# Performance work log

Hardware: AMD Instinct MI355X
Metric: run time of the kernel (lower is better)

The kernel has to match this reference:

```python
import jax, jax.numpy as jnp
import numpy as np

B, C, H, D, W = 1, 32, 32, 32, 32   # batch, channels, 3D grid
M1 = M2 = M3 = 16                   # fourier modes kept per dim
KS = 3                              # spatial attention kernel size
MEM = 5                             # memory slots
EPS = 1e-5
N = H * D * W


def _gelu(x):
    return jax.nn.gelu(x, approximate=False)  # torch exact GELU


def _gn(x):
    # GroupNorm(1, C) without affine: normalize over (C,H,D,W) per sample
    mu = jnp.mean(x, axis=(1, 2, 3, 4), keepdims=True)
    var = jnp.var(x, axis=(1, 2, 3, 4), keepdims=True)
    return (x - mu) * jax.lax.rsqrt(var + EPS)


def _spectral_conv(x, wr, wi):
    # classic 3D FNO spectral conv: keep low modes (4 corner blocks in dims H,D; low block in rfft dim W)
    xf = jnp.fft.rfftn(x, axes=(2, 3, 4))                 # (B,C,H,D,W//2+1) complex64
    w = wr + 1j * wi                                      # (4,Cin,Cout,M1,M2,M3)
    of = jnp.zeros((x.shape[0], C, H, D, W // 2 + 1), xf.dtype)
    corners = [(slice(0, M1), slice(0, M2)), (slice(H - M1, H), slice(0, M2)),
               (slice(0, M1), slice(D - M2, D)), (slice(H - M1, H), slice(D - M2, D))]
    for i, (s1, s2) in enumerate(corners):
        of = of.at[:, :, s1, s2, :M3].set(
            jnp.einsum('bixyz,ioxyz->boxyz', xf[:, :, s1, s2, :M3], w[i]))
    return jnp.fft.irfftn(of, s=(H, D, W), axes=(2, 3, 4))


def _forward(x, t, prev_memory, w_spec_r, w_spec_i, norm1_g, norm1_b,
             mlp_w1, mlp_b1, mlp_w2, mlp_b2, tin_gw, tin_gb, tin_bw, tin_bb,
             q_w, q_b, k_w, k_b, v_w, v_b, mem_key, mem_value,
             gate_w, gate_b, gru_wih, gru_whh, gru_bih, gru_bhh):
    skip1 = x
    skip2 = _gelu(x)
    # spectral conv -> GroupNorm(affine) + residual -> gelu
    h = _spectral_conv(x, w_spec_r, w_spec_i)
    h = _gelu(_gn(h) * norm1_g[None, :, None, None, None]
              + norm1_b[None, :, None, None, None] + skip1)
    # pointwise Conv1d MLP over channels
    hf = h.reshape(B, C, N)
    u = _gelu(jnp.einsum('oc,bcn->bon', mlp_w1, hf) + mlp_b1[None, :, None])
    hf = jnp.einsum('oc,bcn->bon', mlp_w2, u) + mlp_b2[None, :, None]
    h = hf.reshape(B, C, H, D, W)
    # time-conditioned instance norm: gamma/beta from 1x1 conv over t (B,C)
    gamma = (jnp.einsum('oc,bc->bo', tin_gw, t) + tin_gb)[:, :, None, None, None]
    beta = (jnp.einsum('oc,bc->bo', tin_bw, t) + tin_bb)[:, :, None, None, None]
    h = gamma * _gn(h) + beta
    # ---- spatial attention with memory ----
    pad = KS // 2
    xp = jnp.pad(h, ((0, 0), (0, 0), (pad, pad), (pad, pad), (pad, pad)))
    # 3D unfold: (B,C,27,N) patches via 27 shifted views
    patches = jnp.stack([xp[:, :, i:i + H, j:j + D, l:l + W]
                         for i in range(KS) for j in range(KS) for l in range(KS)],
                        axis=2).reshape(B, C, KS ** 3, N)
    hf = h.reshape(B, C, N)
    q = jnp.einsum('oc,bcn->bon', q_w, hf) + q_b[None, :, None]              # (B,C,N)
    k_sp = jnp.einsum('oc,bcmn->bomn', k_w, patches) + k_b[None, :, None, None]
    v_sp = jnp.einsum('oc,bcmn->bomn', v_w, patches) + v_b[None, :, None, None]
    mem_k = jnp.broadcast_to(mem_key[None, :, :, None], (B, C, MEM, N))
    mem_v = jnp.broadcast_to(mem_value[None, :, :, None], (B, C, MEM, N))
    k = jnp.concatenate([mem_k, k_sp], axis=2)                               # (B,C,32,N)
    v = jnp.concatenate([mem_v, v_sp], axis=2)
    attn = jax.nn.softmax(q[:, :, None, :] * k / jnp.sqrt(jnp.float32(C)), axis=2)
    out = jnp.sum(attn * v, axis=2)                                          # (B,C,N)
    cat = jnp.concatenate([hf, out], axis=1)                                 # (B,2C,N)
    gate = jax.nn.sigmoid(jnp.einsum('oc,bcn->bon', gate_w, cat) + gate_b[None, :, None])
    out = gate * out + (1.0 - gate) * hf
    out = out.reshape(B, C, H, D, W)
    # GRUCell memory update from spatially pooled features
    m_in = jnp.mean(out, axis=(2, 3, 4))                                     # (B,C)
    gi = m_in @ gru_wih.T + gru_bih
    gh = prev_memory @ gru_whh.T + gru_bhh
    ir, iz, inn = jnp.split(gi, 3, axis=1)
    hr, hz, hn = jnp.split(gh, 3, axis=1)
    r = jax.nn.sigmoid(ir + hr)
    z = jax.nn.sigmoid(iz + hz)
    n = jnp.tanh(inn + r * hn)
    new_memory = (1.0 - z) * n + z * prev_memory                             # (B,C)
    return out + skip2, new_memory


def setup_inputs():
    key = jax.random.key(0)
    ks = jax.random.split(key, 20)
    def rn(k, shape, s):
        return jax.random.normal(k, shape, jnp.float32) * s
    spec_scale = 1.0 / (C * C)
    return dict(
        x=jax.random.normal(ks[0], (B, C, H, D, W), jnp.float32),
        t=jax.random.normal(ks[1], (B, C), jnp.float32),
        prev_memory=jnp.zeros((B, C), jnp.float32),
        w_spec_r=rn(ks[2], (4, C, C, M1, M2, M3), spec_scale),
        w_spec_i=rn(ks[3], (4, C, C, M1, M2, M3), spec_scale),
        norm1_g=jnp.ones((C,), jnp.float32),
        norm1_b=jnp.zeros((C,), jnp.float32),
        mlp_w1=rn(ks[4], (C // 2, C), 0.1), mlp_b1=jnp.zeros((C // 2,), jnp.float32),
        mlp_w2=rn(ks[5], (C, C // 2), 0.1), mlp_b2=jnp.zeros((C,), jnp.float32),
        tin_gw=rn(ks[6], (C, C), 0.1), tin_gb=jnp.ones((C,), jnp.float32),
        tin_bw=rn(ks[7], (C, C), 0.1), tin_bb=jnp.zeros((C,), jnp.float32),
        q_w=rn(ks[8], (C, C), 0.1), q_b=jnp.zeros((C,), jnp.float32),
        k_w=rn(ks[9], (C, C), 0.1), k_b=jnp.zeros((C,), jnp.float32),
        v_w=rn(ks[10], (C, C), 0.1), v_b=jnp.zeros((C,), jnp.float32),
        mem_key=jax.random.normal(ks[11], (C, MEM), jnp.float32),
        mem_value=jax.random.normal(ks[12], (C, MEM), jnp.float32),
        gate_w=rn(ks[13], (C, 2 * C), 0.1), gate_b=jnp.zeros((C,), jnp.float32),
        gru_wih=rn(ks[14], (3 * C, C), 0.1), gru_whh=rn(ks[15], (3 * C, C), 0.1),
        gru_bih=jnp.zeros((3 * C,), jnp.float32), gru_bhh=jnp.zeros((3 * C,), jnp.float32),
    )


def reference(x, t, prev_memory, w_spec_r, w_spec_i, norm1_g, norm1_b,
              mlp_w1, mlp_b1, mlp_w2, mlp_b2, tin_gw, tin_gb, tin_bw, tin_bb,
              q_w, q_b, k_w, k_b, v_w, v_b, mem_key, mem_value,
              gate_w, gate_b, gru_wih, gru_whh, gru_bih, gru_bhh):
    return _forward(x, t, prev_memory, w_spec_r, w_spec_i, norm1_g, norm1_b,
                    mlp_w1, mlp_b1, mlp_w2, mlp_b2, tin_gw, tin_gb, tin_bw, tin_bb,
                    q_w, q_b, k_w, k_b, v_w, v_b, mem_key, mem_value,
                    gate_w, gate_b, gru_wih, gru_whh, gru_bih, gru_bhh)
```

## Files before the change

kernel.cpp:

```cpp
#include <hip/hip_runtime.h>
#include <hip/hip_bf16.h>
#include <math.h>

#define NSP 32768
#define NZ 17

__device__ __forceinline__ float geluf(float x){
    return 0.5f * x * (1.0f + erff(x * 0.70710678118654752f));
}
__device__ __forceinline__ float sigmoidf_(float x){
    return 1.0f / (1.0f + __expf(-x));
}


__global__ void k_fwd(const float* __restrict__ x, float* __restrict__ Br, float* __restrict__ Bi){
    __shared__ float tile[32*33];
    __shared__ float ar[544], ai[544];
    __shared__ float ct[32], st[32];
    int b = blockIdx.x, t = threadIdx.x;
    if (t < 32){ float ang = 6.283185307179586477f * (float)t / 32.0f; ct[t] = cosf(ang); st[t] = sinf(ang); }
    const float* src = x + b * 1024;
    for (int j = t; j < 1024; j += 256) tile[(j & 31) * 33 + (j >> 5)] = src[j];
    __syncthreads();
    for (int idx = t; idx < 544; idx += 256){
        int d = idx / 17, z = idx - d * 17;
        float sr = 0.f, si = 0.f;
        #pragma unroll
        for (int w = 0; w < 32; ++w){
            int a = (z * w) & 31;
            float v = tile[w * 33 + d];
            sr += v * ct[a];
            si -= v * st[a];
        }
        ar[idx] = sr; ai[idx] = si;
    }
    __syncthreads();
    for (int idx = t; idx < 544; idx += 256){
        int kd = idx / 17, z = idx - kd * 17;
        float sr = 0.f, si = 0.f;
        #pragma unroll
        for (int d = 0; d < 32; ++d){
            int a = (kd * d) & 31;
            float c = ct[a], s = st[a];
            float vr = ar[d * 17 + z], vi = ai[d * 17 + z];
            sr += vr * c + vi * s;
            si += vi * c - vr * s;
        }
        Br[b * 544 + idx] = sr; Bi[b * 544 + idx] = si;
    }
}

__global__ void k_fft_h(const float* __restrict__ Br, const float* __restrict__ Bi,
                        float* __restrict__ Ar, float* __restrict__ Ai){
    __shared__ float ir[544], ii[544];
    __shared__ float ct[32], st[32];
    int b = blockIdx.x, t = threadIdx.x;
    int c = b >> 5, d = b & 31;
    if (t < 32){ float ang = 6.283185307179586477f * (float)t / 32.0f; ct[t] = cosf(ang); st[t] = sinf(ang); }
    for (int j = t; j < 544; j += 256){
        int h = j / 17, z = j - h * 17;
        int g = ((c * 32 + h) * 32 + d) * NZ + z;
        ir[j] = Br[g]; ii[j] = Bi[g];
    }
    __syncthreads();
    for (int idx = t; idx < 544; idx += 256){
        int kh = idx / 17, z = idx - kh * 17;
        float sr = 0.f, si = 0.f;
        #pragma unroll
        for (int h = 0; h < 32; ++h){
            int a = (kh * h) & 31;
            float c2 = ct[a], s2 = st[a];
            float vr = ir[h * 17 + z], vi = ii[h * 17 + z];
            sr += vr * c2 + vi * s2;
            si += vi * c2 - vr * s2;
        }
        int g = ((c * 32 + kh) * 32 + d) * NZ + z;
        Ar[g] = sr; Ai[g] = si;
    }
}

__global__ void k_modemul(const float* __restrict__ Xr, const float* __restrict__ Xi,
                          const float* __restrict__ Wr, const float* __restrict__ Wi,
                          float* __restrict__ Or, float* __restrict__ Oi){
    __shared__ float xr[32 * 64], xi[32 * 64];
    int b = blockIdx.x;
    int corner = b >> 6;
    int xm = (b >> 2) & 15;
    int ymg = b & 3;
    int xg = xm + ((corner & 1) << 4);
    int ybase = ymg * 4 + ((corner >> 1) << 4);
    int t = threadIdx.x;
    for (int idx = t; idx < 2048; idx += 256){
        int i = idx >> 6, m = idx & 63;
        int y = ybase + (m >> 4), z = m & 15;
        int g = ((i * 32 + xg) * 32 + y) * NZ + z;
        xr[idx] = Xr[g]; xi[idx] = Xi[g];
    }
    if (t < 128){
        int o = t >> 2, y = ybase + (t & 3);
        int g = ((o * 32 + xg) * 32 + y) * NZ + 16;
        Or[g] = 0.f; Oi[g] = 0.f;
    }
    __syncthreads();
    int wv = t >> 6, lane = t & 63;
    float ar[8], ai[8];
    #pragma unroll
    for (int oo = 0; oo < 8; ++oo){ ar[oo] = 0.f; ai[oo] = 0.f; }
    int wtail = xm * 256 + ymg * 64 + lane;
    for (int i = 0; i < 32; ++i){
        float vxr = xr[i * 64 + lane], vxi = xi[i * 64 + lane];
        #pragma unroll
        for (int oo = 0; oo < 8; ++oo){
            int o = oo * 4 + wv;
            int addr = ((corner * 32 + i) * 32 + o) * 4096 + wtail;
            float wr = Wr[addr], wi = Wi[addr];
            ar[oo] += wr * vxr - wi * vxi;
            ai[oo] += wr * vxi + wi * vxr;
        }
    }
    int y = ybase + (lane >> 4), z = lane & 15;
    #pragma unroll
    for (int oo = 0; oo < 8; ++oo){
        int o = oo * 4 + wv;
        int g = ((o * 32 + xg) * 32 + y) * NZ + z;
        Or[g] = ar[oo]; Oi[g] = ai[oo];
    }
}

__global__ void k_ifft_h(const float* __restrict__ Br, const float* __restrict__ Bi,
                         float* __restrict__ Ar, float* __restrict__ Ai){
    __shared__ float ir[544], ii[544];
    __shared__ float ct[32], st[32];
    int b = blockIdx.x, t = threadIdx.x;
    int c = b >> 5, y = b & 31;
    if (t < 32){ float ang = 6.283185307179586477f * (float)t / 32.0f; ct[t] = cosf(ang); st[t] = sinf(ang); }
    for (int j = t; j < 544; j += 256){
        int xk = j / 17, z = j - xk * 17;
        int g = ((c * 32 + xk) * 32 + y) * NZ + z;
        ir[j] = Br[g]; ii[j] = Bi[g];
    }
    __syncthreads();
    for (int idx = t; idx < 544; idx += 256){
        int h = idx / 17, z = idx - h * 17;
        float sr = 0.f, si = 0.f;
        #pragma unroll
        for (int k = 0; k < 32; ++k){
            int a = (k * h) & 31;
            float c2 = ct[a], s2 = st[a];
            float vr = ir[k * 17 + z], vi = ii[k * 17 + z];
            sr += vr * c2 - vi * s2;
            si += vr * s2 + vi * c2;
        }
        int g = ((c * 32 + h) * 32 + y) * NZ + z;
        Ar[g] = sr; Ai[g] = si;
    }
}

__global__ void k_inv(const float* __restrict__ Ar, const float* __restrict__ Ai,
                      float* __restrict__ spec,
                      float* __restrict__ psum, float* __restrict__ psq){
    __shared__ float ir[544], ii[544];
    __shared__ float cr[544], ci[544];
    __shared__ float ct[32], st[32];
    __shared__ float ls[256], lq[256];
    int b = blockIdx.x, t = threadIdx.x;
    if (t < 32){ float ang = 6.283185307179586477f * (float)t / 32.0f; ct[t] = cosf(ang); st[t] = sinf(ang); }
    const float* pr = Ar + b * 544;
    const float* pi = Ai + b * 544;
    for (int j = t; j < 544; j += 256){ ir[j] = pr[j]; ii[j] = pi[j]; }
    __syncthreads();
    for (int idx = t; idx < 544; idx += 256){
        int d = idx / 17, z = idx - d * 17;
        float sr = 0.f, si = 0.f;
        #pragma unroll
        for (int k = 0; k < 32; ++k){
            int a = (k * d) & 31;
            float c2 = ct[a], s2 = st[a];
            float vr = ir[k * 17 + z], vi = ii[k * 17 + z];
            sr += vr * c2 - vi * s2;
            si += vr * s2 + vi * c2;
        }
        cr[idx] = sr; ci[idx] = si;
    }
    __syncthreads();
    const float inv = 1.0f / 32768.0f;
    float s_loc = 0.f, q_loc = 0.f;
    for (int idx = t; idx < 1024; idx += 256){
        int d = idx >> 5, w = idx & 31;
        float s = cr[d * 17 + 0] + ((w & 1) ? -cr[d * 17 + 16] : cr[d * 17 + 16]);
        #pragma unroll
        for (int z = 1; z < 16; ++z){
            int a = (z * w) & 31;
            s += 2.0f * (cr[d * 17 + z] * ct[a] - ci[d * 17 + z] * st[a]);
        }
        s *= inv;
        spec[b * 1024 + idx] = s;
        s_loc += s; q_loc += s * s;
    }
    ls[t] = s_loc; lq[t] = q_loc; __syncthreads();
    for (int off = 128; off > 0; off >>= 1){
        if (t < off){ ls[t] += ls[t + off]; lq[t] += lq[t + off]; }
        __syncthreads();
    }
    if (t == 0){ psum[b] = ls[0]; psq[b] = lq[0]; }
}


__global__ void k_finalize1(const float* __restrict__ psum, const float* __restrict__ psq,
                            int n, float* __restrict__ red){
    __shared__ float ls[256], lq[256];
    int t = threadIdx.x;
    float s = 0.f, q = 0.f;
    for (int j = t; j < n; j += 256){ s += psum[j]; q += psq[j]; }
    ls[t] = s; lq[t] = q; __syncthreads();
    for (int off = 128; off > 0; off >>= 1){
        if (t < off){ ls[t] += ls[t + off]; lq[t] += lq[t + off]; }
        __syncthreads();
    }
    if (t == 0){
        float mu = ls[0] * (1.0f / 1048576.0f);
        float var = lq[0] * (1.0f / 1048576.0f) - mu * mu;
        red[0] = mu; red[1] = rsqrtf(var + 1e-5f);
    }
}

__global__ void k_finalize2(const float* __restrict__ psum, const float* __restrict__ psq,
                            int n, const float* __restrict__ tin,
                            const float* __restrict__ tgw, const float* __restrict__ tgb,
                            const float* __restrict__ tbw, const float* __restrict__ tbb,
                            float* __restrict__ red){
    __shared__ float ls[256], lq[256];
    int t = threadIdx.x;
    float s = 0.f, q = 0.f;
    for (int j = t; j < n; j += 256){ s += psum[j]; q += psq[j]; }
    ls[t] = s; lq[t] = q; __syncthreads();
    for (int off = 128; off > 0; off >>= 1){
        if (t < off){ ls[t] += ls[t + off]; lq[t] += lq[t + off]; }
        __syncthreads();
    }
    if (t == 0){
        float mu = ls[0] * (1.0f / 1048576.0f);
        float var = lq[0] * (1.0f / 1048576.0f) - mu * mu;
        red[2] = mu; red[3] = rsqrtf(var + 1e-5f);
    }
    if (t < 64){
        int o = t & 31;
        const float* w = (t < 32) ? tgw : tbw;
        const float* bi = (t < 32) ? tgb : tbb;
        float a = bi[o];
        #pragma unroll
        for (int c = 0; c < 32; ++c) a += w[o * 32 + c] * tin[c];
        red[(t < 32 ? 16 : 48) + o] = a;
    }
}

__global__ void k_mlp(const float* __restrict__ spec, const float* __restrict__ x,
                      const float* __restrict__ n1g, const float* __restrict__ n1b,
                      const float* __restrict__ red,
                      const float* __restrict__ w1, const float* __restrict__ b1,
                      const float* __restrict__ w2, const float* __restrict__ b2,
                      float* __restrict__ h2,
                      float* __restrict__ psum, float* __restrict__ psq){
    __shared__ float W1[512], W2[512], B1[16], B2[32], GG[32], BB[32];
    __shared__ float ls[256], lq[256];
    int t = threadIdx.x;
    for (int j = t; j < 512; j += 256){ W1[j] = w1[j]; W2[j] = w2[j]; }
    if (t < 16) B1[t] = b1[t];
    if (t < 32){ B2[t] = b2[t]; GG[t] = n1g[t]; BB[t] = n1b[t]; }
    __syncthreads();
    float mu = red[0], rs = red[1];
    int n = blockIdx.x * 256 + t;
    float hv[32];
    #pragma unroll
    for (int c = 0; c < 32; ++c){
        float v = (spec[c * NSP + n] - mu) * rs * GG[c] + BB[c] + x[c * NSP + n];
        hv[c] = geluf(v);
    }
    float u[16];
    #pragma unroll
    for (int o = 0; o < 16; ++o){
        float a = B1[o];
        #pragma unroll
        for (int c = 0; c < 32; ++c) a += W1[o * 32 + c] * hv[c];
        u[o] = geluf(a);
    }
    float s_loc = 0.f, q_loc = 0.f;
    #pragma unroll
    for (int o = 0; o < 32; ++o){
        float a = B2[o];
        #pragma unroll
        for (int c = 0; c < 16; ++c) a += W2[o * 16 + c] * u[c];
        h2[o * NSP + n] = a;
        s_loc += a; q_loc += a * a;
    }
    ls[t] = s_loc; lq[t] = q_loc; __syncthreads();
    for (int off = 128; off > 0; off >>= 1){
        if (t < off){ ls[t] += ls[t + off]; lq[t] += lq[t + off]; }
        __syncthreads();
    }
    if (t == 0){ psum[blockIdx.x] = ls[0]; psq[blockIdx.x] = lq[0]; }
}

__global__ void k_qkv(const float* __restrict__ h2, const float* __restrict__ red,
                      const float* __restrict__ qw, const float* __restrict__ qb,
                      const float* __restrict__ kw, const float* __restrict__ vw,
                      float* __restrict__ h3, float* __restrict__ Q,
                      float* __restrict__ KH, float* __restrict__ VH){
    __shared__ float QW[1024], KW[1024], VW[1024], GA[32], BE[32], QB[32];
    int t = threadIdx.x;
    for (int j = t; j < 1024; j += 256){ QW[j] = qw[j]; KW[j] = kw[j]; VW[j] = vw[j]; }
    if (t < 32){ GA[t] = red[16 + t]; BE[t] = red[48 + t]; QB[t] = qb[t]; }
    __syncthreads();
    float mu = red[2], rs = red[3];
    int n = blockIdx.x * 256 + t;
    float hv[32];
    #pragma unroll
    for (int c = 0; c < 32; ++c){
        float v = GA[c] * ((h2[c * NSP + n] - mu) * rs) + BE[c];
        hv[c] = v;
        h3[c * NSP + n] = v;
    }
    #pragma unroll
    for (int o = 0; o < 32; ++o){
        float aq = QB[o], ak = 0.f, av = 0.f;
        #pragma unroll
        for (int c = 0; c < 32; ++c){
            float v = hv[c];
            aq += QW[o * 32 + c] * v;
            ak += KW[o * 32 + c] * v;
            av += VW[o * 32 + c] * v;
        }
        Q[o * NSP + n] = aq;
        KH[o * NSP + n] = ak;
        VH[o * NSP + n] = av;
    }
}

__global__ void k_attn(const float* __restrict__ Q, const float* __restrict__ KH,
                       const float* __restrict__ VH, const float* __restrict__ h3,
                       const float* __restrict__ x,
                       const float* __restrict__ kb, const float* __restrict__ vb,
                       const float* __restrict__ mk, const float* __restrict__ mv,
                       const float* __restrict__ gw, const float* __restrict__ gb,
                       float* __restrict__ outp, float* __restrict__ mpart){
    __shared__ float GWT1[1024], GWT2[1024];
    __shared__ float MK[160], MV[160];
    __shared__ float l_out[256], l_h3[256], l_fin[256];
    int t = threadIdx.x;
    for (int j = t; j < 1024; j += 256){
        int c_ = j & 31, cc_ = j >> 5;
        GWT1[j] = gw[c_ * 64 + cc_];
        GWT2[j] = gw[c_ * 64 + 32 + cc_];
    }
    if (t < 160){ MK[t] = mk[t]; MV[t] = mv[t]; }
    int bid = blockIdx.x;
    int swz = (bid & 7) * 512 + (bid >> 3);
    int c = t >> 3, nl = t & 7;
    int n = swz * 8 + nl;
    int w_ = n & 31, d_ = (n >> 5) & 31, h_ = n >> 10;
    const float scale = 0.17677669529663688f;
    float q = Q[c * NSP + n];
    float kbc = kb[c], vbc = vb[c];
    __syncthreads();
    float s = 0.f, acc = 0.f;
    #pragma unroll
    for (int j = 0; j < 5; ++j){
        float e = __expf(q * MK[c * 5 + j] * scale);
        s += e; acc += e * MV[c * 5 + j];
    }
    int oob = 0;
    for (int di = -1; di <= 1; ++di){
        int hh = h_ + di;
        if ((unsigned)hh >= 32u){ oob += 9; continue; }
        for (int dj = -1; dj <= 1; ++dj){
            int dd = d_ + dj;
            if ((unsigned)dd >= 32u){ oob += 3; continue; }
            int rbase = (hh * 32 + dd) * 32;
            #pragma unroll
            for (int dl = -1; dl <= 1; ++dl){
                int ww = w_ + dl;
                if ((unsigned)ww < 32u){
                    int np = rbase + ww;
                    float k = kbc + KH[c * NSP + np];
                    float v = vbc + VH[c * NSP + np];
                    float e = __expf(q * k * scale);
                    s += e; acc += e * v;
                } else oob++;
            }
        }
    }
    float eb = __expf(q * kbc * scale);
    s += (float)oob * eb; acc += (float)oob * eb * vbc;
    float out0 = acc / s;
    float h3v = h3[c * NSP + n];
    l_out[t] = out0;
    l_h3[t] = h3v;
    __syncthreads();
    float g = gb[c];
    #pragma unroll
    for (int cc = 0; cc < 32; ++cc){
        g += GWT1[cc * 32 + c] * l_h3[cc * 8 + nl] + GWT2[cc * 32 + c] * l_out[cc * 8 + nl];
    }
    g = sigmoidf_(g);
    float fin = g * out0 + (1.0f - g) * h3v;
    l_fin[t] = fin;
    float xo = x[c * NSP + n];
    outp[c * NSP + n] = fin + geluf(xo);
    __syncthreads();
    if (nl == 0){
        float ssum = 0.f;
        #pragma unroll
        for (int j = 0; j < 8; ++j) ssum += l_fin[c * 8 + j];
        mpart[c * 4096 + swz] = ssum;
    }
}

__global__ void k_mred(const float* __restrict__ mpart, float* __restrict__ red){
    __shared__ float ls[256];
    int c = blockIdx.x, t = threadIdx.x;
    const float4* p = (const float4*)(mpart + c * 4096);
    float s = 0.f;
    #pragma unroll
    for (int j = 0; j < 4; ++j){
        float4 v = p[t + j * 256];
        s += v.x + v.y + v.z + v.w;
    }
    ls[t] = s; __syncthreads();
    for (int off = 128; off > 0; off >>= 1){
        if (t < off) ls[t] += ls[t + off];
        __syncthreads();
    }
    if (t == 0) red[128 + c] = ls[0] * (1.0f / 32768.0f);
}

__global__ void k_gru(const float* __restrict__ red, const float* __restrict__ pm,
                      const float* __restrict__ wih, const float* __restrict__ whh,
                      const float* __restrict__ bih, const float* __restrict__ bhh,
                      float* __restrict__ outp){
    __shared__ float m_in[32], gi[96], gh[96];
    int t = threadIdx.x;
    if (t < 32) m_in[t] = red[128 + t];
    __syncthreads();
    if (t < 96){
        float a = bih[t], b2 = bhh[t];
        #pragma unroll
        for (int cc = 0; cc < 32; ++cc){
            a += wih[t * 32 + cc] * m_in[cc];
            b2 += whh[t * 32 + cc] * pm[cc];
        }
        gi[t] = a; gh[t] = b2;
    }
    __syncthreads();
    if (t < 32){
        float r = sigmoidf_(gi[t] + gh[t]);
        float z = sigmoidf_(gi[32 + t] + gh[32 + t]);
        float nn = tanhf(gi[64 + t] + r * gh[64 + t]);
        float nm = (1.0f - z) * nn + z * pm[t];
        outp[1048576 + t] = nm;
    }
}

extern "C" void kernel_launch(void* const* d_in, const int* in_sizes, int n_in,
                              void* d_out, int out_size, void* d_ws, size_t ws_size,
                              hipStream_t stream){
    const float* x   = (const float*)d_in[0];
    const float* tin = (const float*)d_in[1];
    const float* pm  = (const float*)d_in[2];
    const float* wsr = (const float*)d_in[3];
    const float* wsi = (const float*)d_in[4];
    const float* n1g = (const float*)d_in[5];
    const float* n1b = (const float*)d_in[6];
    const float* mw1 = (const float*)d_in[7];
    const float* mb1 = (const float*)d_in[8];
    const float* mw2 = (const float*)d_in[9];
    const float* mb2 = (const float*)d_in[10];
    const float* tgw = (const float*)d_in[11];
    const float* tgb = (const float*)d_in[12];
    const float* tbw = (const float*)d_in[13];
    const float* tbb = (const float*)d_in[14];
    const float* qw  = (const float*)d_in[15];
    const float* qb  = (const float*)d_in[16];
    const float* kw  = (const float*)d_in[17];
    const float* kb  = (const float*)d_in[18];
    const float* vw  = (const float*)d_in[19];
    const float* vb  = (const float*)d_in[20];
    const float* mk  = (const float*)d_in[21];
    const float* mv  = (const float*)d_in[22];
    const float* gw  = (const float*)d_in[23];
    const float* gb  = (const float*)d_in[24];
    const float* wih = (const float*)d_in[25];
    const float* whh = (const float*)d_in[26];
    const float* bih = (const float*)d_in[27];
    const float* bhh = (const float*)d_in[28];

    float* ws = (float*)d_ws;
    float* Ar   = ws + 0;
    float* Ai   = ws + 557056;
    float* Br   = ws + 1114112;
    float* Bi   = ws + 1671168;
    float* spec = ws + 2228224;
    float* h1   = ws + 3276800;
    float* h2   = ws + 4325376;
    float* h3   = ws + 5373952;
    float* red  = ws + 6422528;
    float* psum = ws + 6422784;
    float* psq  = ws + 6423808;
    float* Qb  = Br;
    float* KHb = spec;
    float* VHb = h1;
    float* mpart = Ar;

    float* outp = (float*)d_out;

    k_fwd    <<<1024, 256, 0, stream>>>(x, Br, Bi);
    k_fft_h  <<<1024, 256, 0, stream>>>(Br, Bi, Ar, Ai);
    k_modemul<<<256, 256, 0, stream>>>(Ar, Ai, wsr, wsi, Br, Bi);
    k_ifft_h <<<1024, 256, 0, stream>>>(Br, Bi, Ar, Ai);
    k_inv    <<<1024, 256, 0, stream>>>(Ar, Ai, spec, psum, psq);
    k_finalize1<<<1, 256, 0, stream>>>(psum, psq, 1024, red);
    k_mlp    <<<128, 256, 0, stream>>>(spec, x, n1g, n1b, red, mw1, mb1, mw2, mb2, h2, psum, psq);
    k_finalize2<<<1, 256, 0, stream>>>(psum, psq, 128, tin, tgw, tgb, tbw, tbb, red);
    k_qkv    <<<128, 256, 0, stream>>>(h2, red, qw, qb, kw, vw, h3, Qb, KHb, VHb);
    k_attn   <<<4096, 256, 0, stream>>>(Qb, KHb, VHb, h3, x, kb, vb, mk, mv, gw, gb, outp, mpart);
    k_mred   <<<32, 256, 0, stream>>>(mpart, red);
    k_gru    <<<1, 128, 0, stream>>>(red, pm, wih, whh, bih, bhh, outp);
}
```

Baseline: 197.7 us.

## Split attention into LDS-tiled neighbourhood kernel and separate per-point gate kernel

The fused attention kernel is split in two. The attention kernel now assigns one (channel, h-plane) pair per block and stages the three neighbouring K/V planes in shared memory, so the 27-point stencil reads LDS instead of repeatedly gathering from global memory. A new gate kernel keeps all 32 channels per spatial point in registers and computes the channel-mixing gate, the output and per-block channel sums for the memory mean. This adds an extra global round trip for the attention output and uses only 128 blocks for the gate kernel, which may leave many CUs idle.

```diff
diff --git a/kernel.cpp b/kernel.cpp
--- a/kernel.cpp
+++ b/kernel.cpp
@@ -337,96 +337,121 @@
 }
 
 __global__ void k_attn(const float* __restrict__ Q, const float* __restrict__ KH,
-                       const float* __restrict__ VH, const float* __restrict__ h3,
-                       const float* __restrict__ x,
+                       const float* __restrict__ VH,
                        const float* __restrict__ kb, const float* __restrict__ vb,
                        const float* __restrict__ mk, const float* __restrict__ mv,
+                       float* __restrict__ out0){
+    __shared__ float KL[3][1024], VL[3][1024];
+    int bid = blockIdx.x;
+    int swz = (bid & 7) * 128 + (bid >> 3);
+    int c = swz >> 5, h_ = swz & 31;
+    int t = threadIdx.x;
+    #pragma unroll
+    for (int p = 0; p < 3; ++p){
+        int hh = h_ - 1 + p;
+        if ((unsigned)hh < 32u){
+            const float* sk = KH + (c * 32 + hh) * 1024;
+            const float* sv = VH + (c * 32 + hh) * 1024;
+            for (int j = t; j < 1024; j += 256){ KL[p][j] = sk[j]; VL[p][j] = sv[j]; }
+        }
+    }
+    float kbc = kb[c], vbc = vb[c];
+    float mkv[5], mvv[5];
+    #pragma unroll
+    for (int j = 0; j < 5; ++j){ mkv[j] = mk[c * 5 + j]; mvv[j] = mv[c * 5 + j]; }
+    float qv[4];
+    #pragma unroll
+    for (int i = 0; i < 4; ++i) qv[i] = Q[c * NSP + h_ * 1024 + i * 256 + t];
+    __syncthreads();
+    const float scale = 0.17677669529663688f;
+    #pragma unroll
+    for (int i = 0; i < 4; ++i){
+        int nl = i * 256 + t;
+        int d_ = nl >> 5, w_ = nl & 31;
+        float q = qv[i];
+        float s = 0.f, acc = 0.f;
+        #pragma unroll
+        for (int j = 0; j < 5; ++j){
+            float e = __expf(q * mkv[j] * scale);
+            s += e; acc += e * mvv[j];
+        }
+        int oob = 0;
+        #pragma unroll
+        for (int p = 0; p < 3; ++p){
+            int hh = h_ - 1 + p;
+            if ((unsigned)hh >= 32u){ oob += 9; continue; }
+            #pragma unroll
+            for (int dj = -1; dj <= 1; ++dj){
+                int dd = d_ + dj;
+                if ((unsigned)dd >= 32u){ oob += 3; continue; }
+                int rb = dd * 32;
+                #pragma unroll
+                for (int dl = -1; dl <= 1; ++dl){
+                    int ww = w_ + dl;
+                    if ((unsigned)ww < 32u){
+                        float k = kbc + KL[p][rb + ww];
+                        float v = vbc + VL[p][rb + ww];
+                        float e = __expf(q * k * scale);
+                        s += e; acc += e * v;
+                    } else oob++;
+                }
+            }
+        }
+        float eb = __expf(q * kbc * scale);
+        s += (float)oob * eb; acc += (float)oob * eb * vbc;
+        out0[c * NSP + h_ * 1024 + nl] = acc / s;
+    }
+}
+
+__global__ void k_gate(const float* __restrict__ h3, const float* __restrict__ out0,
+                       const float* __restrict__ x,
                        const float* __restrict__ gw, const float* __restrict__ gb,
                        float* __restrict__ outp, float* __restrict__ mpart){
-    __shared__ float GWT1[1024], GWT2[1024];
-    __shared__ float MK[160], MV[160];
-    __shared__ float l_out[256], l_h3[256], l_fin[256];
-    int t = threadIdx.x;
-    for (int j = t; j < 1024; j += 256){
-        int c_ = j & 31, cc_ = j >> 5;
-        GWT1[j] = gw[c_ * 64 + cc_];
-        GWT2[j] = gw[c_ * 64 + 32 + cc_];
-    }
-    if (t < 160){ MK[t] = mk[t]; MV[t] = mv[t]; }
-    int bid = blockIdx.x;
-    int swz = (bid & 7) * 512 + (bid >> 3);
-    int c = t >> 3, nl = t & 7;
-    int n = swz * 8 + nl;
-    int w_ = n & 31, d_ = (n >> 5) & 31, h_ = n >> 10;
-    const float scale = 0.17677669529663688f;
-    float q = Q[c * NSP + n];
-    float kbc = kb[c], vbc = vb[c];
-    __syncthreads();
-    float s = 0.f, acc = 0.f;
-    #pragma unroll
-    for (int j = 0; j < 5; ++j){
-        float e = __expf(q * MK[c * 5 + j] * scale);
-        s += e; acc += e * MV[c * 5 + j];
-    }
-    int oob = 0;
-    for (int di = -1; di <= 1; ++di){
-        int hh = h_ + di;
-        if ((unsigned)hh >= 32u){ oob += 9; continue; }
-        for (int dj = -1; dj <= 1; ++dj){
-            int dd = d_ + dj;
-            if ((unsigned)dd >= 32u){ oob += 3; continue; }
-            int rbase = (hh * 32 + dd) * 32;
-            #pragma unroll
-            for (int dl = -1; dl <= 1; ++dl){
-                int ww = w_ + dl;
-                if ((unsigned)ww < 32u){
-                    int np = rbase + ww;
-                    float k = kbc + KH[c * NSP + np];
-                    float v = vbc + VH[c * NSP + np];
-                    float e = __expf(q * k * scale);
-                    s += e; acc += e * v;
-                } else oob++;
-            }
-        }
-    }
-    float eb = __expf(q * kbc * scale);
-    s += (float)oob * eb; acc += (float)oob * eb * vbc;
-    float out0 = acc / s;
-    float h3v = h3[c * NSP + n];
-    l_out[t] = out0;
-    l_h3[t] = h3v;
-    __syncthreads();
-    float g = gb[c];
-    #pragma unroll
-    for (int cc = 0; cc < 32; ++cc){
-        g += GWT1[cc * 32 + c] * l_h3[cc * 8 + nl] + GWT2[cc * 32 + c] * l_out[cc * 8 + nl];
-    }
-    g = sigmoidf_(g);
-    float fin = g * out0 + (1.0f - g) * h3v;
-    l_fin[t] = fin;
-    float xo = x[c * NSP + n];
-    outp[c * NSP + n] = fin + geluf(xo);
-    __syncthreads();
-    if (nl == 0){
-        float ssum = 0.f;
-        #pragma unroll
-        for (int j = 0; j < 8; ++j) ssum += l_fin[c * 8 + j];
-        mpart[c * 4096 + swz] = ssum;
+    __shared__ float GW[2048];
+    __shared__ float FT[32 * 264];
+    __shared__ float PS[256];
+    int t = threadIdx.x;
+    for (int j = t; j < 2048; j += 256) GW[j] = gw[j];
+    int n = blockIdx.x * 256 + t;
+    float hv[32], ov[32];
+    #pragma unroll
+    for (int c = 0; c < 32; ++c){ hv[c] = h3[c * NSP + n]; ov[c] = out0[c * NSP + n]; }
+    __syncthreads();
+    #pragma unroll
+    for (int c = 0; c < 32; ++c){
+        float g = gb[c];
+        #pragma unroll
+        for (int cc = 0; cc < 32; ++cc){
+            g += GW[c * 64 + cc] * hv[cc] + GW[c * 64 + 32 + cc] * ov[cc];
+        }
+        g = sigmoidf_(g);
+        float fin = g * ov[c] + (1.0f - g) * hv[c];
+        FT[c * 264 + t] = fin;
+        outp[c * NSP + n] = fin + geluf(x[c * NSP + n]);
+    }
+    __syncthreads();
+    {
+        int c8 = t >> 3, seg = t & 7;
+        float s = 0.f;
+        #pragma unroll
+        for (int j = 0; j < 32; ++j) s += FT[c8 * 264 + seg * 32 + j];
+        PS[t] = s;
+    }
+    __syncthreads();
+    if (t < 32){
+        float s = 0.f;
+        #pragma unroll
+        for (int j = 0; j < 8; ++j) s += PS[t * 8 + j];
+        mpart[t * 128 + blockIdx.x] = s;
     }
 }
 
 __global__ void k_mred(const float* __restrict__ mpart, float* __restrict__ red){
-    __shared__ float ls[256];
+    __shared__ float ls[128];
     int c = blockIdx.x, t = threadIdx.x;
-    const float4* p = (const float4*)(mpart + c * 4096);
-    float s = 0.f;
-    #pragma unroll
-    for (int j = 0; j < 4; ++j){
-        float4 v = p[t + j * 256];
-        s += v.x + v.y + v.z + v.w;
-    }
-    ls[t] = s; __syncthreads();
-    for (int off = 128; off > 0; off >>= 1){
+    ls[t] = mpart[c * 128 + t];
+    __syncthreads();
+    for (int off = 64; off > 0; off >>= 1){
         if (t < off) ls[t] += ls[t + off];
         __syncthreads();
     }
@@ -505,10 +530,11 @@
     float* red  = ws + 6422528;
     float* psum = ws + 6422784;
     float* psq  = ws + 6423808;
-    float* Qb  = Br;
-    float* KHb = spec;
-    float* VHb = h1;
-    float* mpart = Ar;
+    float* Qb   = Br;
+    float* KHb  = spec;
+    float* VHb  = h1;
+    float* out0 = Ar;
+    float* mpart = h2;
 
     float* outp = (float*)d_out;
 
@@ -521,7 +547,8 @@
     k_mlp    <<<128, 256, 0, stream>>>(spec, x, n1g, n1b, red, mw1, mb1, mw2, mb2, h2, psum, psq);
     k_finalize2<<<1, 256, 0, stream>>>(psum, psq, 128, tin, tgw, tgb, tbw, tbb, red);
     k_qkv    <<<128, 256, 0, stream>>>(h2, red, qw, qb, kw, vw, h3, Qb, KHb, VHb);
-    k_attn   <<<4096, 256, 0, stream>>>(Qb, KHb, VHb, h3, x, kb, vb, mk, mv, gw, gb, outp, mpart);
-    k_mred   <<<32, 256, 0, stream>>>(mpart, red);
+    k_attn   <<<1024, 256, 0, stream>>>(Qb, KHb, VHb, kb, vb, mk, mv, out0);
+    k_gate   <<<128, 256, 0, stream>>>(h3, out0, x, gw, gb, outp, mpart);
+    k_mred   <<<32, 128, 0, stream>>>(mpart, red);
     k_gru    <<<1, 128, 0, stream>>>(red, pm, wih, whh, bih, bhh, outp);
 }
```

Measured after the change: 194.1 us. Within noise of the previous version (-1.8%).
